# Optimization experiments

Hardware: AMD Instinct MI355X
Metric: run time of the kernel (lower is better)

Reference implementation:

```python
import jax, jax.numpy as jnp
import numpy as np

BN_EPS = 1e-5

def setup_inputs() -> dict:
    key = jax.random.key(0)
    ks = jax.random.split(key, 7)
    B, D, A = 16384, 768, 51
    s = 1.0 / np.sqrt(D)
    return {
        "x": jax.random.normal(ks[0], (B, D), dtype=jnp.float32),
        "W_embed": jax.random.uniform(ks[1], (D, D), minval=-s, maxval=s, dtype=jnp.float32),
        "b_embed": jax.random.uniform(ks[2], (D,), minval=-s, maxval=s, dtype=jnp.float32),
        "W_attr": jax.random.uniform(ks[3], (A, D), minval=-s, maxval=s, dtype=jnp.float32),  # stacked per-attribute (dim->1) heads
        "b_attr": jax.random.uniform(ks[4], (A,), minval=-s, maxval=s, dtype=jnp.float32),
        "gamma": jnp.ones((A,), dtype=jnp.float32),
        "beta": jnp.zeros((A,), dtype=jnp.float32),
    }

def reference(x, W_embed, b_embed, W_attr, b_attr, gamma, beta):
    # word_embed: Linear(dim, dim)
    h = x @ W_embed.T + b_embed                      # [B, D]
    # fused per-attribute heads: cat of attr_num (dim->1) linears == one (dim->attr_num) matmul
    logits = h @ W_attr.T + b_attr                    # [B, A]
    # BatchNorm1d (training mode: batch statistics, biased variance)
    mean = jnp.mean(logits, axis=0)
    var = jnp.var(logits, axis=0)
    y = (logits - mean) * jax.lax.rsqrt(var + BN_EPS) * gamma + beta
    return y
```

## Files before the change

### kernel.cpp

```cpp
#include <hip/hip_runtime.h>
#include <hip/hip_bf16.h>

typedef _Float16 halfx8 __attribute__((ext_vector_type(8)));
typedef _Float16 halfx4 __attribute__((ext_vector_type(4)));
typedef float floatx4 __attribute__((ext_vector_type(4)));

#define GLOBAL_AS __attribute__((address_space(1)))
#define LDS_AS __attribute__((address_space(3)))

__device__ __forceinline__ void async_copy_16(const void* g, void* l) {
    __builtin_amdgcn_global_load_lds((GLOBAL_AS void*)g, (LDS_AS void*)l, 16, 0, 0);
}

#define PM 16384
#define PD 768
#define PA 51


__global__ __launch_bounds__(256) void init_kernel(
    const float* __restrict__ Wa, const float* __restrict__ b_embed,
    const float* __restrict__ b_attr,
    float* __restrict__ wc32, float* __restrict__ bc, float* __restrict__ stats)
{
    int b = blockIdx.x, t = threadIdx.x;
    if (b < 12) {
        #pragma unroll
        for (int j = 0; j < 4; ++j)
            ((float4*)wc32)[b * 1024 + j * 256 + t] = (float4){0.f, 0.f, 0.f, 0.f};
    } else {
        if (t < 128) stats[t] = 0.f;
        __shared__ float red[256];
        int a = t & 63, qtr = t >> 6;
        float partial = 0.f;
        if (a < PA) {
            const float* war = Wa + (size_t)a * PD + qtr * 192;
            const float* ber = b_embed + qtr * 192;
            #pragma unroll 4
            for (int k = 0; k < 192; k += 4) {
                floatx4 w = *(const floatx4*)(war + k);
                floatx4 e = *(const floatx4*)(ber + k);
                partial += w[0]*e[0] + w[1]*e[1] + w[2]*e[2] + w[3]*e[3];
            }
        }
        red[t] = partial;
        __syncthreads();
        if (t < PA)
            bc[t] = red[t] + red[64 + t] + red[128 + t] + red[192 + t] + b_attr[t];
    }
}

__global__ __launch_bounds__(256) void wcomb_kernel(
    const float* __restrict__ We, const float* __restrict__ Wa,
    float* __restrict__ wc32)
{
    __shared__ float WeS[48 * 64];
    __shared__ float WaS[51 * 48];
    const int b = blockIdx.x;
    const int kc = b & 15;
    const int nc = b >> 4;
    const int k0 = kc * 48, d0 = nc * 64;
    const int t = threadIdx.x;

    #pragma unroll
    for (int j = 0; j < 3; ++j) {
        int idx4 = j * 256 + t;
        int r = idx4 >> 4, c4 = idx4 & 15;
        *(floatx4*)&WeS[r * 64 + c4 * 4] =
            *(const floatx4*)(We + (size_t)(k0 + r) * PD + d0 + c4 * 4);
    }
    for (int idx4 = t; idx4 < 612; idx4 += 256) {
        int r = idx4 / 12, c4 = idx4 % 12;
        *(floatx4*)&WaS[r * 48 + c4 * 4] =
            *(const floatx4*)(Wa + (size_t)r * PD + k0 + c4 * 4);
    }
    __syncthreads();

    const int c = t & 63;
    const int ag = t >> 6;

    float we[48];
    #pragma unroll
    for (int k = 0; k < 48; ++k) we[k] = WeS[k * 64 + c];

    #pragma unroll
    for (int i = 0; i < 13; ++i) {
        int a = ag + i * 4;
        if (a < PA) {
            float acc = 0.f;
            #pragma unroll
            for (int k4 = 0; k4 < 12; ++k4) {
                floatx4 wa = *(const floatx4*)&WaS[a * 48 + k4 * 4];
                acc += wa[0] * we[k4*4] + wa[1] * we[k4*4+1]
                     + wa[2] * we[k4*4+2] + wa[3] * we[k4*4+3];
            }
            atomicAdd(&wc32[(size_t)a * PD + d0 + c], acc);
        }
    }
}

__global__ __launch_bounds__(256) void skinny_gemm_kernel(
    const float* __restrict__ X,
    const float* __restrict__ Wc,
    const float* __restrict__ bc,
    float* __restrict__ logits,
    float* __restrict__ stats)
{
    __shared__ float As[32 * 64];
    __shared__ float Bs[64 * 64];
    __shared__ float s_sum[64];
    __shared__ float s_ssq[64];

    const int tid = threadIdx.x;
    const int wave = tid >> 6;
    const int lane = tid & 63;
    const int quad = lane >> 4;
    const int l16 = lane & 15;
    const int wr = wave & 1;
    const int wn = wave >> 1;
    const int row0 = blockIdx.x * 32;

    if (tid < 64) { s_sum[tid] = 0.f; s_ssq[tid] = 0.f; }

    const int g_r  = lane >> 4;
    const int g_sl = lane & 15;

    floatx4 acc[2];
    acc[0] = (floatx4){0.f, 0.f, 0.f, 0.f};
    acc[1] = (floatx4){0.f, 0.f, 0.f, 0.f};

    for (int kt = 0; kt < PD; kt += 64) {
        #pragma unroll
        for (int j = 0; j < 2; ++j) {
            int g = wave * 2 + j;
            int r = g * 4 + g_r;
            int csrc = g_sl ^ (r & 7);
            async_copy_16(X + (size_t)(row0 + r) * PD + kt + csrc * 4, &As[g * 256]);
        }
        #pragma unroll
        for (int j = 0; j < 4; ++j) {
            int g = wave * 4 + j;
            int r = g * 4 + g_r;
            int csrc = g_sl ^ (r & 7);
            async_copy_16(Wc + (size_t)r * PD + kt + csrc * 4, &Bs[g * 256]);
        }
        __syncthreads();
        #pragma unroll
        for (int ks = 0; ks < 2; ++ks) {
            int c0 = ks * 8 + quad * 2;
            int sw = l16 & 7;
            int rA = wr * 16 + l16;
            floatx4 p0 = *(const floatx4*)&As[rA * 64 + ((c0 ^ sw) << 2)];
            floatx4 p1 = *(const floatx4*)&As[rA * 64 + (((c0 + 1) ^ sw) << 2)];
            halfx8 af;
            af[0] = (_Float16)p0[0]; af[1] = (_Float16)p0[1];
            af[2] = (_Float16)p0[2]; af[3] = (_Float16)p0[3];
            af[4] = (_Float16)p1[0]; af[5] = (_Float16)p1[1];
            af[6] = (_Float16)p1[2]; af[7] = (_Float16)p1[3];
            #pragma unroll
            for (int ni = 0; ni < 2; ++ni) {
                int rB = wn * 32 + ni * 16 + l16;
                floatx4 q0 = *(const floatx4*)&Bs[rB * 64 + ((c0 ^ sw) << 2)];
                floatx4 q1 = *(const floatx4*)&Bs[rB * 64 + (((c0 + 1) ^ sw) << 2)];
                halfx8 bf;
                bf[0] = (_Float16)q0[0]; bf[1] = (_Float16)q0[1];
                bf[2] = (_Float16)q0[2]; bf[3] = (_Float16)q0[3];
                bf[4] = (_Float16)q1[0]; bf[5] = (_Float16)q1[1];
                bf[6] = (_Float16)q1[2]; bf[7] = (_Float16)q1[3];
                acc[ni] = __builtin_amdgcn_mfma_f32_16x16x32_f16(af, bf, acc[ni], 0, 0, 0);
            }
        }
        __syncthreads();
    }

    #pragma unroll
    for (int ni = 0; ni < 2; ++ni) {
        int col = wn * 32 + ni * 16 + l16;
        if (col < PA) {
            float bv = bc[col];
            float ps = 0.f, pss = 0.f;
            int rowb = row0 + wr * 16 + quad * 4;
            #pragma unroll
            for (int r = 0; r < 4; ++r) {
                float v = acc[ni][r] + bv;
                logits[(size_t)(rowb + r) * PA + col] = v;
                ps += v; pss += v * v;
            }
            atomicAdd(&s_sum[col], ps);
            atomicAdd(&s_ssq[col], pss);
        }
    }
    __syncthreads();
    if (tid < PA) {
        atomicAdd(&stats[tid], s_sum[tid]);
        atomicAdd(&stats[64 + tid], s_ssq[tid]);
    }
}

__global__ void bn_finalize_kernel(const float* __restrict__ logits,
                                   const float* __restrict__ stats,
                                   const float* __restrict__ gamma,
                                   const float* __restrict__ beta,
                                   float* __restrict__ out, int total) {
    __shared__ float s_scale[PA];
    __shared__ float s_shift[PA];
    int t = threadIdx.x;
    if (t < PA) {
        const float invB = 1.0f / (float)PM;
        float mean = stats[t] * invB;
        float var = stats[64 + t] * invB - mean * mean;
        float inv = rsqrtf(var + 1e-5f);
        float g = gamma[t] * inv;
        s_scale[t] = g;
        s_shift[t] = beta[t] - mean * g;
    }
    __syncthreads();
    int idx = blockIdx.x * 256 + t;
    if (idx < total) {
        int col = idx % PA;
        out[idx] = logits[idx] * s_scale[col] + s_shift[col];
    }
}

extern "C" void kernel_launch(void* const* d_in, const int* in_sizes, int n_in,
                              void* d_out, int out_size, void* d_ws, size_t ws_size,
                              hipStream_t stream) {
    const float* x       = (const float*)d_in[0];
    const float* W_embed = (const float*)d_in[1];
    const float* b_embed = (const float*)d_in[2];
    const float* W_attr  = (const float*)d_in[3];
    const float* b_attr  = (const float*)d_in[4];
    const float* gamma   = (const float*)d_in[5];
    const float* beta    = (const float*)d_in[6];
    float* out = (float*)d_out;

    char* ws = (char*)d_ws;
    float* wc32   = (float*)(ws);
    float* bc     = (float*)(ws + 196608);
    float* stats  = (float*)(ws + 196864);
    float* logits = (float*)(ws + 197376);

    init_kernel<<<13, 256, 0, stream>>>(W_attr, b_embed, b_attr, wc32, bc, stats);
    wcomb_kernel<<<192, 256, 0, stream>>>(W_embed, W_attr, wc32);
    skinny_gemm_kernel<<<512, 256, 0, stream>>>(x, wc32, bc, logits, stats);
    bn_finalize_kernel<<<3264, 256, 0, stream>>>(logits, stats, gamma, beta, out, PM * PA);
}
```

Baseline: 131.3 us.

## Fuse all stages into one cooperative kernel with grid syncs

Merges the four launches (init, weight combine, skinny GEMM, BN finalize) into a single cooperative kernel that separates the phases with grid.sync(). Logits stay in registers across the statistics reduction, so the intermediate logits buffer is never written to or re-read from global memory. The weight-combine phase is also restructured to compute each Wa·We row directly without atomics. In exchange, it depends on all 512 blocks being co-resident for the cooperative launch, adds two grid-wide barriers, and the new combine phase reads We with strided, uncached-looking column accesses.

```diff
diff --git a/kernel.cpp b/kernel.cpp
--- a/kernel.cpp
+++ b/kernel.cpp
@@ -1,8 +1,9 @@
 #include <hip/hip_runtime.h>
-#include <hip/hip_bf16.h>
+#include <hip/hip_cooperative_groups.h>
+
+namespace cg = cooperative_groups;
 
 typedef _Float16 halfx8 __attribute__((ext_vector_type(8)));
-typedef _Float16 halfx4 __attribute__((ext_vector_type(4)));
 typedef float floatx4 __attribute__((ext_vector_type(4)));
 
 #define GLOBAL_AS __attribute__((address_space(1)))
@@ -17,20 +18,54 @@
 #define PA 51
 
 
-__global__ __launch_bounds__(256) void init_kernel(
-    const float* __restrict__ Wa, const float* __restrict__ b_embed,
+__global__ __launch_bounds__(256) void mega_kernel(
+    const float* __restrict__ X,
+    const float* __restrict__ We,
+    const float* __restrict__ Wa,
+    const float* __restrict__ b_embed,
     const float* __restrict__ b_attr,
-    float* __restrict__ wc32, float* __restrict__ bc, float* __restrict__ stats)
+    const float* __restrict__ gamma,
+    const float* __restrict__ beta,
+    float* __restrict__ out,
+    float* __restrict__ wc32,
+    float* __restrict__ bc,
+    float* __restrict__ stats)
 {
-    int b = blockIdx.x, t = threadIdx.x;
-    if (b < 12) {
-        #pragma unroll
-        for (int j = 0; j < 4; ++j)
-            ((float4*)wc32)[b * 1024 + j * 256 + t] = (float4){0.f, 0.f, 0.f, 0.f};
-    } else {
-        if (t < 128) stats[t] = 0.f;
-        __shared__ float red[256];
-        int a = t & 63, qtr = t >> 6;
+    __shared__ __align__(16) char smem[25088];
+    float* WaS   = (float*)smem;
+    float* red   = (float*)(smem + 3072);
+    float* As    = (float*)smem;
+    float* Bs    = (float*)(smem + 8192);
+    float* s_sum = (float*)(smem + 24576);
+    float* s_ssq = (float*)(smem + 24832);
+
+    cg::grid_group grid = cg::this_grid();
+    const int tid = threadIdx.x;
+    const int b = blockIdx.x;
+
+    if (b < 306) {
+        int a = b / 6;
+        int nc = b - a * 6;
+        int d0 = nc * 128;
+        if (tid < 192)
+            *(floatx4*)&WaS[tid * 4] = *(const floatx4*)(Wa + (size_t)a * PD + tid * 4);
+        __syncthreads();
+        int c = tid & 127, h = tid >> 7;
+        const float* wep = We + (size_t)(h * 384) * PD + d0 + c;
+        float acc = 0.f;
+        #pragma unroll 8
+        for (int k = 0; k < 384; ++k)
+            acc += WaS[h * 384 + k] * wep[(size_t)k * PD];
+        red[tid] = acc;
+        __syncthreads();
+        if (h == 0)
+            wc32[(size_t)a * PD + d0 + c] = red[c] + red[128 + c];
+    } else if (b < 319) {
+        int row = PA + (b - 306);
+        for (int i = tid; i < PD; i += 256) wc32[(size_t)row * PD + i] = 0.f;
+    } else if (b == 319) {
+        if (tid < 128) stats[tid] = 0.f;
+        int a = tid & 63, qtr = tid >> 6;
         float partial = 0.f;
         if (a < PA) {
             const float* war = Wa + (size_t)a * PD + qtr * 192;
@@ -42,82 +77,21 @@
                 partial += w[0]*e[0] + w[1]*e[1] + w[2]*e[2] + w[3]*e[3];
             }
         }
-        red[t] = partial;
-        __syncthreads();
-        if (t < PA)
-            bc[t] = red[t] + red[64 + t] + red[128 + t] + red[192 + t] + b_attr[t];
-    }
-}
-
-__global__ __launch_bounds__(256) void wcomb_kernel(
-    const float* __restrict__ We, const float* __restrict__ Wa,
-    float* __restrict__ wc32)
-{
-    __shared__ float WeS[48 * 64];
-    __shared__ float WaS[51 * 48];
-    const int b = blockIdx.x;
-    const int kc = b & 15;
-    const int nc = b >> 4;
-    const int k0 = kc * 48, d0 = nc * 64;
-    const int t = threadIdx.x;
-
-    #pragma unroll
-    for (int j = 0; j < 3; ++j) {
-        int idx4 = j * 256 + t;
-        int r = idx4 >> 4, c4 = idx4 & 15;
-        *(floatx4*)&WeS[r * 64 + c4 * 4] =
-            *(const floatx4*)(We + (size_t)(k0 + r) * PD + d0 + c4 * 4);
-    }
-    for (int idx4 = t; idx4 < 612; idx4 += 256) {
-        int r = idx4 / 12, c4 = idx4 % 12;
-        *(floatx4*)&WaS[r * 48 + c4 * 4] =
-            *(const floatx4*)(Wa + (size_t)r * PD + k0 + c4 * 4);
-    }
-    __syncthreads();
-
-    const int c = t & 63;
-    const int ag = t >> 6;
-
-    float we[48];
-    #pragma unroll
-    for (int k = 0; k < 48; ++k) we[k] = WeS[k * 64 + c];
-
-    #pragma unroll
-    for (int i = 0; i < 13; ++i) {
-        int a = ag + i * 4;
-        if (a < PA) {
-            float acc = 0.f;
-            #pragma unroll
-            for (int k4 = 0; k4 < 12; ++k4) {
-                floatx4 wa = *(const floatx4*)&WaS[a * 48 + k4 * 4];
-                acc += wa[0] * we[k4*4] + wa[1] * we[k4*4+1]
-                     + wa[2] * we[k4*4+2] + wa[3] * we[k4*4+3];
-            }
-            atomicAdd(&wc32[(size_t)a * PD + d0 + c], acc);
-        }
-    }
-}
-
-__global__ __launch_bounds__(256) void skinny_gemm_kernel(
-    const float* __restrict__ X,
-    const float* __restrict__ Wc,
-    const float* __restrict__ bc,
-    float* __restrict__ logits,
-    float* __restrict__ stats)
-{
-    __shared__ float As[32 * 64];
-    __shared__ float Bs[64 * 64];
-    __shared__ float s_sum[64];
-    __shared__ float s_ssq[64];
-
-    const int tid = threadIdx.x;
+        red[tid] = partial;
+        __syncthreads();
+        if (tid < PA)
+            bc[tid] = red[tid] + red[64 + tid] + red[128 + tid] + red[192 + tid] + b_attr[tid];
+    }
+
+    grid.sync();
+
     const int wave = tid >> 6;
     const int lane = tid & 63;
     const int quad = lane >> 4;
     const int l16 = lane & 15;
     const int wr = wave & 1;
     const int wn = wave >> 1;
-    const int row0 = blockIdx.x * 32;
+    const int row0 = b * 32;
 
     if (tid < 64) { s_sum[tid] = 0.f; s_ssq[tid] = 0.f; }
 
@@ -141,7 +115,7 @@
             int g = wave * 4 + j;
             int r = g * 4 + g_r;
             int csrc = g_sl ^ (r & 7);
-            async_copy_16(Wc + (size_t)r * PD + kt + csrc * 4, &Bs[g * 256]);
+            async_copy_16(wc32 + (size_t)r * PD + kt + csrc * 4, &Bs[g * 256]);
         }
         __syncthreads();
         #pragma unroll
@@ -178,11 +152,10 @@
         if (col < PA) {
             float bv = bc[col];
             float ps = 0.f, pss = 0.f;
-            int rowb = row0 + wr * 16 + quad * 4;
             #pragma unroll
             for (int r = 0; r < 4; ++r) {
                 float v = acc[ni][r] + bv;
-                logits[(size_t)(rowb + r) * PA + col] = v;
+                acc[ni][r] = v;
                 ps += v; pss += v * v;
             }
             atomicAdd(&s_sum[col], ps);
@@ -194,30 +167,29 @@
         atomicAdd(&stats[tid], s_sum[tid]);
         atomicAdd(&stats[64 + tid], s_ssq[tid]);
     }
-}
-
-__global__ void bn_finalize_kernel(const float* __restrict__ logits,
-                                   const float* __restrict__ stats,
-                                   const float* __restrict__ gamma,
-                                   const float* __restrict__ beta,
-                                   float* __restrict__ out, int total) {
-    __shared__ float s_scale[PA];
-    __shared__ float s_shift[PA];
-    int t = threadIdx.x;
-    if (t < PA) {
+
+    grid.sync();
+
+    if (tid < PA) {
         const float invB = 1.0f / (float)PM;
-        float mean = stats[t] * invB;
-        float var = stats[64 + t] * invB - mean * mean;
+        float mean = stats[tid] * invB;
+        float var = stats[64 + tid] * invB - mean * mean;
         float inv = rsqrtf(var + 1e-5f);
-        float g = gamma[t] * inv;
-        s_scale[t] = g;
-        s_shift[t] = beta[t] - mean * g;
+        float g = gamma[tid] * inv;
+        s_sum[tid] = g;
+        s_ssq[tid] = beta[tid] - mean * g;
     }
     __syncthreads();
-    int idx = blockIdx.x * 256 + t;
-    if (idx < total) {
-        int col = idx % PA;
-        out[idx] = logits[idx] * s_scale[col] + s_shift[col];
+    #pragma unroll
+    for (int ni = 0; ni < 2; ++ni) {
+        int col = wn * 32 + ni * 16 + l16;
+        if (col < PA) {
+            float sc = s_sum[col], sh = s_ssq[col];
+            int rowb = row0 + wr * 16 + quad * 4;
+            #pragma unroll
+            for (int r = 0; r < 4; ++r)
+                out[(size_t)(rowb + r) * PA + col] = acc[ni][r] * sc + sh;
+        }
     }
 }
 
@@ -234,13 +206,13 @@
     float* out = (float*)d_out;
 
     char* ws = (char*)d_ws;
-    float* wc32   = (float*)(ws);
-    float* bc     = (float*)(ws + 196608);
-    float* stats  = (float*)(ws + 196864);
-    float* logits = (float*)(ws + 197376);
-
-    init_kernel<<<13, 256, 0, stream>>>(W_attr, b_embed, b_attr, wc32, bc, stats);
-    wcomb_kernel<<<192, 256, 0, stream>>>(W_embed, W_attr, wc32);
-    skinny_gemm_kernel<<<512, 256, 0, stream>>>(x, wc32, bc, logits, stats);
-    bn_finalize_kernel<<<3264, 256, 0, stream>>>(logits, stats, gamma, beta, out, PM * PA);
+    float* wc32  = (float*)(ws);
+    float* bc    = (float*)(ws + 196608);
+    float* stats = (float*)(ws + 196864);
+
+    void* args[] = { (void*)&x, (void*)&W_embed, (void*)&W_attr, (void*)&b_embed,
+                     (void*)&b_attr, (void*)&gamma, (void*)&beta, (void*)&out,
+                     (void*)&wc32, (void*)&bc, (void*)&stats };
+    hipLaunchCooperativeKernel((const void*)mega_kernel, dim3(512), dim3(256),
+                               args, 0, stream);
 }
```

Measured after the change: 245.4 us. +86.9%, slower.
